# Kernel optimization log

Measured on AMD Instinct MI355X. Metric: run time of the kernel, lower is better.

## Reference

```python
import jax, jax.numpy as jnp
import numpy as np

NUM_NODES = 100_000
NUM_EDGES = 3_200_000
NUM_GRAPHS = 1_000


def setup_inputs() -> dict:
    key = jax.random.key(0)
    ks = jax.random.split(key, 10)
    x = jax.random.normal(ks[0], (NUM_NODES, 3), dtype=jnp.float32)
    edge_index = jax.random.randint(ks[1], (2, NUM_EDGES), 0, NUM_NODES, dtype=jnp.int64)
    edge_attr = jax.random.normal(ks[2], (NUM_EDGES, 1), dtype=jnp.float32)
    batch = jnp.sort(jax.random.randint(ks[3], (NUM_NODES,), 0, NUM_GRAPHS, dtype=jnp.int64))
    # parameters (Glorot-ish scale)
    W1 = jax.random.normal(ks[4], (3, 16), dtype=jnp.float32) * (1.0 / np.sqrt(3))
    b1 = jnp.zeros((16,), dtype=jnp.float32)
    W2 = jax.random.normal(ks[5], (16, 16), dtype=jnp.float32) * (1.0 / np.sqrt(16))
    b2 = jnp.zeros((16,), dtype=jnp.float32)
    Wl = jax.random.normal(ks[6], (16, 7), dtype=jnp.float32) * (1.0 / np.sqrt(16))
    bl = jnp.zeros((7,), dtype=jnp.float32)
    return {"x": x, "edge_index": edge_index, "edge_attr": edge_attr, "batch": batch,
            "W1": W1, "b1": b1, "W2": W2, "b2": b2, "Wl": Wl, "bl": bl}


def _gcn_conv(h, W, b, row, col, norm, num_nodes):
    # PyG GCNConv: h' = scatter_add(norm * (hW)[row] -> col) + b
    m = (h @ W)[row] * norm[:, None]                      # [E+N, d_out]
    out = jax.ops.segment_sum(m, col, num_segments=num_nodes)
    return out + b


def reference(x, edge_index, edge_attr, batch, W1, b1, W2, b2, Wl, bl):
    num_nodes = x.shape[0]
    # add self loops (GCNConv default), edge weight 1
    loops = jnp.arange(num_nodes, dtype=edge_index.dtype)
    row = jnp.concatenate([edge_index[0], loops])
    col = jnp.concatenate([edge_index[1], loops])
    # symmetric normalization: deg over target (col)
    deg = jax.ops.segment_sum(jnp.ones_like(col, dtype=x.dtype), col, num_segments=num_nodes)
    dis = jnp.where(deg > 0, jax.lax.rsqrt(deg), 0.0)
    norm = dis[row] * dis[col]                            # [E+N]

    h = _gcn_conv(x, W1, b1, row, col, norm, num_nodes)
    h = jax.nn.relu(h)
    h = _gcn_conv(h, W2, b2, row, col, norm, num_nodes)
    # global_add_pool
    g = jax.ops.segment_sum(h, batch, num_segments=NUM_GRAPHS)  # [G, 16]
    logits = g @ Wl + bl                                  # [G, 7]
    return jax.nn.log_softmax(logits, axis=1)
```

## Files before the change

### kernel.cpp

```cpp
#include <hip/hip_runtime.h>
#include <math.h>

#define CHUNK 8192
#define BSH 8
#define BNODES 256
#define RAWCAP 9216
#define MAXCELL 512


union H2 { unsigned int u; _Float16 h[2]; };

__global__ __launch_bounds__(1024) void k_bin(
                      const int* __restrict__ row, const int* __restrict__ col,
                      int* __restrict__ temp, unsigned short* __restrict__ off,
                      int E, int NBLK, int nb) {
    __shared__ int cnt[512];
    __shared__ int cur[512];
    __shared__ int wsum[8];
    __shared__ int stage[CHUNK];
    int blk = blockIdx.x;
    int start = blk * CHUNK;
    int cs = E - start; if (cs > CHUNK) cs = CHUNK;
    int t = threadIdx.x;
    int wid = t >> 6, lane = t & 63;
    if (t < 512) cnt[t] = 0;
    __syncthreads();
    for (int i = t; i < cs; i += 1024) atomicAdd(&cnt[col[start + i] >> BSH], 1);
    __syncthreads();
    if (t < 512) {
        int c = cnt[t];
        int incl = c;
        for (int o = 1; o < 64; o <<= 1) {
            int u = __shfl_up(incl, o, 64);
            if (lane >= o) incl += u;
        }
        if (lane == 63) wsum[wid] = incl;
        cnt[t] = incl - c;
    }
    __syncthreads();
    if (t < 512) {
        int wb = 0;
        for (int i = 0; i < wid; ++i) wb += wsum[i];
        int excl = cnt[t] + wb;
        if (t < nb) off[t * NBLK + blk] = (unsigned short)excl;
        if (t == 0) off[nb * NBLK + blk] = (unsigned short)cs;
        cur[t] = excl;
    }
    __syncthreads();
    for (int i = t; i < cs; i += 1024) {
        int cc = col[start + i];
        int rr = row[start + i];
        int p = atomicAdd(&cur[cc >> BSH], 1);
        stage[p] = (rr << BSH) | (cc & (BNODES - 1));
    }
    __syncthreads();
    for (int i = t; i < cs; i += 1024) temp[start + i] = stage[i];
}

__global__ __launch_bounds__(256) void k_base2(
                       const unsigned short* __restrict__ off, int* __restrict__ base,
                       int* __restrict__ ptrS, float* __restrict__ g,
                       int NBLK, int nbp1, int N, int G16) {
    int gw = (blockIdx.x * 256 + threadIdx.x) >> 6;
    int lane = threadIdx.x & 63;
    if (gw < nbp1) {
        const unsigned short* orow = off + (size_t)gw * NBLK;
        int s = 0;
        for (int ch = lane; ch < NBLK; ch += 64) s += orow[ch];
        for (int o = 32; o > 0; o >>= 1) s += __shfl_down(s, o, 64);
        if (lane == 0) {
            base[gw] = s;
            if (gw == nbp1 - 1) ptrS[N] = s;
        }
    }
    int tid = blockIdx.x * 256 + threadIdx.x;
    for (int i = tid; i < G16; i += gridDim.x * 256) g[i] = 0.0f;
}

__global__ __launch_bounds__(1024) void k_build(
                        const int* __restrict__ temp, const unsigned short* __restrict__ off,
                        const int* __restrict__ base, int* __restrict__ ptrS,
                        float* __restrict__ dinv, int* __restrict__ csr,
                        const float* __restrict__ x, const float* __restrict__ W1,
                        unsigned int* __restrict__ h0u, int NBLK, int N) {
    __shared__ int cnt[BNODES];
    __shared__ int cur[BNODES];
    __shared__ int cellstart[MAXCELL];
    __shared__ int soff[MAXCELL];
    __shared__ int wsum[16];
    __shared__ float sdinv[BNODES];
    __shared__ int raw[RAWCAP];
    __shared__ int stage[RAWCAP];
    int b = blockIdx.x;
    int t = threadIdx.x;
    int wid = t >> 6, lane = t & 63;
    if (t < BNODES) cnt[t] = 0;
    int len0 = 0;
    if (t < MAXCELL) {
        int s0v = 0;
        if (t < NBLK) {
            s0v = (int)off[b * NBLK + t];
            len0 = (int)off[(b + 1) * NBLK + t] - s0v;
        }
        soff[t] = s0v;
        int v = len0;
        for (int o = 1; o < 64; o <<= 1) {
            int u = __shfl_up(v, o, 64);
            if (lane >= o) v += u;
        }
        if (lane == 63) wsum[wid] = v;
        cellstart[t] = v - len0;
    }
    __syncthreads();
    if (t < MAXCELL) {
        int wb = 0;
        for (int i = 0; i < wid; ++i) wb += wsum[i];
        cellstart[t] += wb;
    }
    __syncthreads();
    int bb = base[b];
    int total = base[b + 1] - bb;
    int grp = t >> 4, gl = t & 15;
    for (int cell = grp; cell < NBLK; cell += 64) {
        int s0 = soff[cell];
        int rb = cellstart[cell];
        int len = ((cell + 1 < NBLK) ? cellstart[cell + 1] : total) - rb;
        const int* src = temp + cell * CHUNK + s0;
        for (int j = gl; j < len; j += 16) {
            int e = src[j];
            atomicAdd(&cnt[e & (BNODES - 1)], 1);
            int idx = rb + j;
            if (idx < RAWCAP) raw[idx] = e;
        }
    }
    __syncthreads();
    int c = 0, sincl = 0;
    if (t < BNODES) {
        c = cnt[t];
        sincl = c;
        for (int o = 1; o < 64; o <<= 1) {
            int u = __shfl_up(sincl, o, 64);
            if (lane >= o) sincl += u;
        }
        if (lane == 63) wsum[wid] = sincl;
    }
    __syncthreads();
    if (t < BNODES) {
        int wb2 = 0;
        for (int i = 0; i < wid; ++i) wb2 += wsum[i];
        int lstart = sincl - c + wb2;
        int node = (b << BSH) + t;
        float dv = rsqrtf(1.0f + (float)c);
        sdinv[t] = dv;
        if (node < N) {
            ptrS[node] = bb + lstart;
            dinv[node] = dv;
        }
        cur[t] = lstart;
    }
    __syncthreads();
    int cap = total > RAWCAP ? RAWCAP : total;
    for (int i = t; i < cap; i += 1024) {
        int e = raw[i];
        int p = atomicAdd(&cur[e & (BNODES - 1)], 1);
        int r = e >> BSH;
        if (p < RAWCAP) stage[p] = r;
        else            csr[bb + p] = r;
    }
    if (total > RAWCAP) {
        for (int cell = grp; cell < NBLK; cell += 64) {
            int s0 = soff[cell];
            int rb = cellstart[cell];
            int len = ((cell + 1 < NBLK) ? cellstart[cell + 1] : total) - rb;
            const int* src = temp + cell * CHUNK + s0;
            for (int j = gl; j < len; j += 16) {
                if (rb + j >= RAWCAP) {
                    int e = src[j];
                    int p = atomicAdd(&cur[e & (BNODES - 1)], 1);
                    int r = e >> BSH;
                    if (p < RAWCAP) stage[p] = r;
                    else            csr[bb + p] = r;
                }
            }
        }
    }
    __syncthreads();
    for (int i = t; i < cap; i += 1024) csr[bb + i] = stage[i];
    for (int i = t; i < BNODES * 8; i += 1024) {
        int vl = i >> 3, k2 = i & 7, k = k2 * 2;
        int v = (b << BSH) + vl;
        if (v < N) {
            float x0 = x[v * 3 + 0], x1 = x[v * 3 + 1], x2 = x[v * 3 + 2];
            float d = sdinv[vl];
            H2 p;
            p.h[0] = (_Float16)(d * (x0 * W1[k]     + x1 * W1[16 + k]     + x2 * W1[32 + k]));
            p.h[1] = (_Float16)(d * (x0 * W1[k + 1] + x1 * W1[16 + k + 1] + x2 * W1[32 + k + 1]));
            h0u[v * 8 + k2] = p.u;
        }
    }
}

__global__ void k_gather1(const int* __restrict__ ptrS, const int* __restrict__ csr,
                          const float* __restrict__ dinv, const unsigned int* __restrict__ h0u,
                          const float* __restrict__ W2, const float* __restrict__ b1,
                          unsigned int* __restrict__ h1u, int N) {
    __shared__ float sW[256];
    sW[threadIdx.x] = W2[threadIdx.x];
    __syncthreads();
    int t = blockIdx.x * blockDim.x + threadIdx.x;
    int v = t >> 3, gl = t & 7, k = gl * 2;
    if (v >= N) return;
    int s = ptrS[v], e = ptrS[v + 1];
    float al0 = 0.0f, ah0 = 0.0f, al1 = 0.0f, ah1 = 0.0f;
    int i = s;
    for (; i + 7 < e; i += 8) {
        int myr = __builtin_nontemporal_load(csr + i + gl);
#pragma unroll
        for (int q = 0; q < 8; ++q) {
            int r = __shfl(myr, q, 8);
            H2 p; p.u = h0u[r * 8 + gl];
            if (q & 1) { al1 += (float)p.h[0]; ah1 += (float)p.h[1]; }
            else       { al0 += (float)p.h[0]; ah0 += (float)p.h[1]; }
        }
    }
    if (i < e) {
        int rem = e - i;
        int myr = (gl < rem) ? __builtin_nontemporal_load(csr + i + gl) : 0;
        for (int q = 0; q < rem; ++q) {
            int r = __shfl(myr, q, 8);
            H2 p; p.u = h0u[r * 8 + gl];
            al0 += (float)p.h[0]; ah0 += (float)p.h[1];
        }
    }
    H2 selfp; selfp.u = h0u[v * 8 + gl];
    float d = dinv[v];
    float h_lo = fmaxf(d * (al0 + al1 + (float)selfp.h[0]) + b1[k], 0.0f);
    float h_hi = fmaxf(d * (ah0 + ah1 + (float)selfp.h[1]) + b1[k + 1], 0.0f);
    float o0 = 0.0f, o1 = 0.0f;
#pragma unroll
    for (int j = 0; j < 8; ++j) {
        float hl = __shfl(h_lo, j, 8);
        float hh = __shfl(h_hi, j, 8);
        o0 += hl * sW[(2 * j) * 16 + k]     + hh * sW[(2 * j + 1) * 16 + k];
        o1 += hl * sW[(2 * j) * 16 + k + 1] + hh * sW[(2 * j + 1) * 16 + k + 1];
    }
    H2 outp;
    outp.h[0] = (_Float16)(d * o0);
    outp.h[1] = (_Float16)(d * o1);
    __builtin_nontemporal_store(outp.u, h1u + v * 8 + gl);
}

__global__ void k_gather2(const int* __restrict__ ptrS, const int* __restrict__ csr,
                          const float* __restrict__ dinv, const unsigned int* __restrict__ h1u,
                          const float* __restrict__ b2, const int* __restrict__ batch,
                          float* __restrict__ g, int N) {
    int t = blockIdx.x * blockDim.x + threadIdx.x;
    int v = t >> 3, gl = t & 7, k = gl * 2;
    bool valid = (v < N);
    float val0 = 0.0f, val1 = 0.0f;
    int bg = 0;
    if (valid) {
        int s = ptrS[v], e = ptrS[v + 1];
        float al0 = 0.0f, ah0 = 0.0f, al1 = 0.0f, ah1 = 0.0f;
        int i = s;
        for (; i + 7 < e; i += 8) {
            int myr = __builtin_nontemporal_load(csr + i + gl);
#pragma unroll
            for (int q = 0; q < 8; ++q) {
                int r = __shfl(myr, q, 8);
                H2 p; p.u = h1u[r * 8 + gl];
                if (q & 1) { al1 += (float)p.h[0]; ah1 += (float)p.h[1]; }
                else       { al0 += (float)p.h[0]; ah0 += (float)p.h[1]; }
            }
        }
        if (i < e) {
            int rem = e - i;
            int myr = (gl < rem) ? __builtin_nontemporal_load(csr + i + gl) : 0;
            for (int q = 0; q < rem; ++q) {
                int r = __shfl(myr, q, 8);
                H2 p; p.u = h1u[r * 8 + gl];
                al0 += (float)p.h[0]; ah0 += (float)p.h[1];
            }
        }
        H2 selfp; selfp.u = h1u[v * 8 + gl];
        float d = dinv[v];
        val0 = d * (al0 + al1 + (float)selfp.h[0]) + b2[k];
        val1 = d * (ah0 + ah1 + (float)selfp.h[1]) + b2[k + 1];
        bg = batch[v];
    }
    int lane = threadIdx.x & 63;
    int bg0 = __shfl(bg, lane & 7, 64);
    bool uni = __all(valid && (bg == bg0));
    if (uni) {
        val0 += __shfl_xor(val0, 8, 64);
        val0 += __shfl_xor(val0, 16, 64);
        val0 += __shfl_xor(val0, 32, 64);
        val1 += __shfl_xor(val1, 8, 64);
        val1 += __shfl_xor(val1, 16, 64);
        val1 += __shfl_xor(val1, 32, 64);
        if (lane < 8) {
            atomicAdd(&g[bg * 16 + k], val0);
            atomicAdd(&g[bg * 16 + k + 1], val1);
        }
    } else if (valid) {
        atomicAdd(&g[bg * 16 + k], val0);
        atomicAdd(&g[bg * 16 + k + 1], val1);
    }
}

__global__ void k_head(const float* __restrict__ g, const float* __restrict__ Wl,
                       const float* __restrict__ bl, float* __restrict__ out, int G) {
    int gi = blockIdx.x * blockDim.x + threadIdx.x;
    if (gi >= G) return;
    float gv[16];
#pragma unroll
    for (int k = 0; k < 16; ++k) gv[k] = g[gi * 16 + k];
    float lo[7];
    float mx = -1e30f;
#pragma unroll
    for (int j = 0; j < 7; ++j) {
        float a = bl[j];
#pragma unroll
        for (int k = 0; k < 16; ++k) a += gv[k] * Wl[k * 7 + j];
        lo[j] = a;
        mx = fmaxf(mx, a);
    }
    float s = 0.0f;
#pragma unroll
    for (int j = 0; j < 7; ++j) s += expf(lo[j] - mx);
    float lse = mx + logf(s);
#pragma unroll
    for (int j = 0; j < 7; ++j) out[gi * 7 + j] = lo[j] - lse;
}

extern "C" void kernel_launch(void* const* d_in, const int* in_sizes, int n_in,
                              void* d_out, int out_size, void* d_ws, size_t ws_size,
                              hipStream_t stream) {
    const float* x    = (const float*)d_in[0];
    const int*   ei   = (const int*)d_in[1];
    const int*   batch = (const int*)d_in[3];
    const float* W1 = (const float*)d_in[4];
    const float* b1 = (const float*)d_in[5];
    const float* W2 = (const float*)d_in[6];
    const float* b2 = (const float*)d_in[7];
    const float* Wl = (const float*)d_in[8];
    const float* bl = (const float*)d_in[9];
    float* out = (float*)d_out;

    const int N = in_sizes[0] / 3;
    const int E = in_sizes[1] / 2;
    const int G = out_size / 7;

    const int* row = ei;
    const int* col = ei + E;

    const int NBLK = (E + CHUNK - 1) / CHUNK;
    const int nb   = (N + BNODES - 1) >> BSH;

    int* w = (int*)d_ws;
    float* dinv = (float*)w;            w += N;
    int*   ptrS = w;                    w += N + 1;
    int*   base = w;                    w += nb + 1;
    unsigned short* off = (unsigned short*)w;
    w += ((nb + 1) * NBLK + 1) / 2;
    int*   csr  = w;                    w += E;
    int*   temp = w;                    w += E;
    unsigned int* h0u = (unsigned int*)w;  w += 8 * N;
    unsigned int* h1u = (unsigned int*)w;  w += 8 * N;
    float* g    = (float*)w;            w += 16 * G;

    const int TB = 256;
    const int n8  = N * 8;
    const int G16 = G * 16;
    const int nbp1 = nb + 1;
    const int baseBlocks = (nbp1 * 64 + 255) / 256;

    k_bin<<<NBLK, 1024, 0, stream>>>(row, col, temp, off, E, NBLK, nb);
    k_base2<<<baseBlocks, 256, 0, stream>>>(off, base, ptrS, g, NBLK, nbp1, N, G16);
    k_build<<<nb, 1024, 0, stream>>>(temp, off, base, ptrS, dinv, csr, x, W1, h0u, NBLK, N);
    k_gather1<<<(n8 + TB - 1) / TB, TB, 0, stream>>>(ptrS, csr, dinv, h0u, W2, b1, h1u, N);
    k_gather2<<<(n8 + TB - 1) / TB, TB, 0, stream>>>(ptrS, csr, dinv, h1u, b2, batch, g, N);
    k_head<<<(G + TB - 1) / TB, TB, 0, stream>>>(g, Wl, bl, out, G);
}
```

Before: 193.2 us.

## Fold base-offset kernel into build and fuse head into last gather block

Removes the k_base2 launch. Each k_build block now recomputes its base offset by reducing its own row of per-chunk offsets, and zeroing of the pooled buffer moves into k_bin. The classifier head runs inside k_gather2, in whichever block takes the last ticket on a global atomic counter. This cuts two kernel launches and their gaps, at the cost of a threadfence and ticket atomic in every gather2 block, plus a serial head computation done by a single block.

```diff
diff --git a/kernel.cpp b/kernel.cpp
--- a/kernel.cpp
+++ b/kernel.cpp
@@ -13,16 +13,19 @@
 __global__ __launch_bounds__(1024) void k_bin(
                       const int* __restrict__ row, const int* __restrict__ col,
                       int* __restrict__ temp, unsigned short* __restrict__ off,
-                      int E, int NBLK, int nb) {
+                      float* __restrict__ g, int* __restrict__ cnt1,
+                      int E, int NBLK, int nb, int G16) {
     __shared__ int cnt[512];
     __shared__ int cur[512];
-    __shared__ int wsum[8];
+    __shared__ int wsum[16];
     __shared__ int stage[CHUNK];
     int blk = blockIdx.x;
     int start = blk * CHUNK;
     int cs = E - start; if (cs > CHUNK) cs = CHUNK;
     int t = threadIdx.x;
     int wid = t >> 6, lane = t & 63;
+    for (int i = blk * 1024 + t; i < G16; i += gridDim.x * 1024) g[i] = 0.0f;
+    if (blk == 0 && t == 0) atomicExch(cnt1, 0);
     if (t < 512) cnt[t] = 0;
     __syncthreads();
     for (int i = t; i < cs; i += 1024) atomicAdd(&cnt[col[start + i] >> BSH], 1);
@@ -57,47 +60,27 @@
     for (int i = t; i < cs; i += 1024) temp[start + i] = stage[i];
 }
 
-__global__ __launch_bounds__(256) void k_base2(
-                       const unsigned short* __restrict__ off, int* __restrict__ base,
-                       int* __restrict__ ptrS, float* __restrict__ g,
-                       int NBLK, int nbp1, int N, int G16) {
-    int gw = (blockIdx.x * 256 + threadIdx.x) >> 6;
-    int lane = threadIdx.x & 63;
-    if (gw < nbp1) {
-        const unsigned short* orow = off + (size_t)gw * NBLK;
-        int s = 0;
-        for (int ch = lane; ch < NBLK; ch += 64) s += orow[ch];
-        for (int o = 32; o > 0; o >>= 1) s += __shfl_down(s, o, 64);
-        if (lane == 0) {
-            base[gw] = s;
-            if (gw == nbp1 - 1) ptrS[N] = s;
-        }
-    }
-    int tid = blockIdx.x * 256 + threadIdx.x;
-    for (int i = tid; i < G16; i += gridDim.x * 256) g[i] = 0.0f;
-}
-
 __global__ __launch_bounds__(1024) void k_build(
                         const int* __restrict__ temp, const unsigned short* __restrict__ off,
-                        const int* __restrict__ base, int* __restrict__ ptrS,
-                        float* __restrict__ dinv, int* __restrict__ csr,
+                        int* __restrict__ ptrS, float* __restrict__ dinv,
+                        int* __restrict__ csr,
                         const float* __restrict__ x, const float* __restrict__ W1,
-                        unsigned int* __restrict__ h0u, int NBLK, int N) {
+                        unsigned int* __restrict__ h0u, int NBLK, int N, int nb) {
     __shared__ int cnt[BNODES];
     __shared__ int cur[BNODES];
     __shared__ int cellstart[MAXCELL];
     __shared__ int soff[MAXCELL];
     __shared__ int wsum[16];
     __shared__ float sdinv[BNODES];
+    __shared__ int s_bb, s_total;
     __shared__ int raw[RAWCAP];
     __shared__ int stage[RAWCAP];
     int b = blockIdx.x;
     int t = threadIdx.x;
     int wid = t >> 6, lane = t & 63;
     if (t < BNODES) cnt[t] = 0;
-    int len0 = 0;
+    int len0 = 0, s0v = 0;
     if (t < MAXCELL) {
-        int s0v = 0;
         if (t < NBLK) {
             s0v = (int)off[b * NBLK + t];
             len0 = (int)off[(b + 1) * NBLK + t] - s0v;
@@ -117,9 +100,21 @@
         for (int i = 0; i < wid; ++i) wb += wsum[i];
         cellstart[t] += wb;
     }
-    __syncthreads();
-    int bb = base[b];
-    int total = base[b + 1] - bb;
+    if (t == NBLK - 1) s_total = cellstart[t] + len0;
+    __syncthreads();
+    int sv = s0v;
+    for (int o = 32; o > 0; o >>= 1) sv += __shfl_down(sv, o, 64);
+    if (lane == 0 && wid < 8) wsum[wid] = sv;
+    __syncthreads();
+    if (t == 0) {
+        int bbl = 0;
+        for (int i = 0; i < 8; ++i) bbl += wsum[i];
+        s_bb = bbl;
+    }
+    __syncthreads();
+    int bb = s_bb;
+    int total = s_total;
+    if (b == nb - 1 && t == 0) ptrS[N] = bb + total;
     int grp = t >> 4, gl = t & 15;
     for (int cell = grp; cell < NBLK; cell += 64) {
         int s0 = soff[cell];
@@ -253,7 +248,10 @@
 __global__ void k_gather2(const int* __restrict__ ptrS, const int* __restrict__ csr,
                           const float* __restrict__ dinv, const unsigned int* __restrict__ h1u,
                           const float* __restrict__ b2, const int* __restrict__ batch,
-                          float* __restrict__ g, int N) {
+                          float* __restrict__ g, const float* __restrict__ Wl,
+                          const float* __restrict__ bl, float* __restrict__ out,
+                          int* __restrict__ cnt1, int N, int G) {
+    __shared__ int s_ticket;
     int t = blockIdx.x * blockDim.x + threadIdx.x;
     int v = t >> 3, gl = t & 7, k = gl * 2;
     bool valid = (v < N);
@@ -306,31 +304,34 @@
         atomicAdd(&g[bg * 16 + k], val0);
         atomicAdd(&g[bg * 16 + k + 1], val1);
     }
-}
-
-__global__ void k_head(const float* __restrict__ g, const float* __restrict__ Wl,
-                       const float* __restrict__ bl, float* __restrict__ out, int G) {
-    int gi = blockIdx.x * blockDim.x + threadIdx.x;
-    if (gi >= G) return;
-    float gv[16];
-#pragma unroll
-    for (int k = 0; k < 16; ++k) gv[k] = g[gi * 16 + k];
-    float lo[7];
-    float mx = -1e30f;
-#pragma unroll
-    for (int j = 0; j < 7; ++j) {
-        float a = bl[j];
-#pragma unroll
-        for (int k = 0; k < 16; ++k) a += gv[k] * Wl[k * 7 + j];
-        lo[j] = a;
-        mx = fmaxf(mx, a);
-    }
-    float s = 0.0f;
-#pragma unroll
-    for (int j = 0; j < 7; ++j) s += expf(lo[j] - mx);
-    float lse = mx + logf(s);
-#pragma unroll
-    for (int j = 0; j < 7; ++j) out[gi * 7 + j] = lo[j] - lse;
+    __threadfence();
+    __syncthreads();
+    if (threadIdx.x == 0) s_ticket = atomicAdd(cnt1, 1);
+    __syncthreads();
+    if (s_ticket == (int)gridDim.x - 1) {
+        __threadfence();
+        for (int gi = threadIdx.x; gi < G; gi += blockDim.x) {
+            float gv[16];
+#pragma unroll
+            for (int kk = 0; kk < 16; ++kk) gv[kk] = atomicAdd(&g[gi * 16 + kk], 0.0f);
+            float lo[7];
+            float mx = -1e30f;
+#pragma unroll
+            for (int j = 0; j < 7; ++j) {
+                float a = bl[j];
+#pragma unroll
+                for (int kk = 0; kk < 16; ++kk) a += gv[kk] * Wl[kk * 7 + j];
+                lo[j] = a;
+                mx = fmaxf(mx, a);
+            }
+            float ssum = 0.0f;
+#pragma unroll
+            for (int j = 0; j < 7; ++j) ssum += expf(lo[j] - mx);
+            float lse = mx + logf(ssum);
+#pragma unroll
+            for (int j = 0; j < 7; ++j) out[gi * 7 + j] = lo[j] - lse;
+        }
+    }
 }
 
 extern "C" void kernel_launch(void* const* d_in, const int* in_sizes, int n_in,
@@ -360,7 +361,6 @@
     int* w = (int*)d_ws;
     float* dinv = (float*)w;            w += N;
     int*   ptrS = w;                    w += N + 1;
-    int*   base = w;                    w += nb + 1;
     unsigned short* off = (unsigned short*)w;
     w += ((nb + 1) * NBLK + 1) / 2;
     int*   csr  = w;                    w += E;
@@ -368,17 +368,15 @@
     unsigned int* h0u = (unsigned int*)w;  w += 8 * N;
     unsigned int* h1u = (unsigned int*)w;  w += 8 * N;
     float* g    = (float*)w;            w += 16 * G;
+    int*   cnt1 = w;                    w += 1;
 
     const int TB = 256;
     const int n8  = N * 8;
     const int G16 = G * 16;
-    const int nbp1 = nb + 1;
-    const int baseBlocks = (nbp1 * 64 + 255) / 256;
-
-    k_bin<<<NBLK, 1024, 0, stream>>>(row, col, temp, off, E, NBLK, nb);
-    k_base2<<<baseBlocks, 256, 0, stream>>>(off, base, ptrS, g, NBLK, nbp1, N, G16);
-    k_build<<<nb, 1024, 0, stream>>>(temp, off, base, ptrS, dinv, csr, x, W1, h0u, NBLK, N);
+
+    k_bin<<<NBLK, 1024, 0, stream>>>(row, col, temp, off, g, cnt1, E, NBLK, nb, G16);
+    k_build<<<nb, 1024, 0, stream>>>(temp, off, ptrS, dinv, csr, x, W1, h0u, NBLK, N, nb);
     k_gather1<<<(n8 + TB - 1) / TB, TB, 0, stream>>>(ptrS, csr, dinv, h0u, W2, b1, h1u, N);
-    k_gather2<<<(n8 + TB - 1) / TB, TB, 0, stream>>>(ptrS, csr, dinv, h1u, b2, batch, g, N);
-    k_head<<<(G + TB - 1) / TB, TB, 0, stream>>>(g, Wl, bl, out, G);
-}
+    k_gather2<<<(n8 + TB - 1) / TB, TB, 0, stream>>>(ptrS, csr, dinv, h1u, b2, batch,
+                                                     g, Wl, bl, out, cnt1, N, G);
+}
```

After: 463.9 us. +140.1%, slower.
